# Kernel optimization log

Measured on AMD Instinct MI355X. Metric: run time of the kernel, lower is better.

The kernel has to match this reference:

```python
import jax, jax.numpy as jnp
import numpy as np

H = 4      # SSM / attn heads (d_model/headdim = 256/64)
WIN = 4    # attention window over bands


def _ln(x, g, b):
    m = jnp.mean(x, -1, keepdims=True)
    v = jnp.mean((x - m) ** 2, -1, keepdims=True)
    return (x - m) * jax.lax.rsqrt(v + 1e-5) * g + b


def setup_inputs() -> dict:
    key = jax.random.key(0)
    ks = jax.random.split(key, 24)
    def rn(i, shape, s=0.05):
        return jax.random.normal(ks[i], shape, jnp.float32) * s
    B, T, K, D = 2, 256, 8, 256
    return {
        "z": rn(0, (B, T, K, D), 1.0),
        "ln1_g": jnp.ones((D,), jnp.float32), "ln1_b": jnp.zeros((D,), jnp.float32),
        "Wx": rn(1, (D, D)), "conv_w": rn(2, (D, 4), 0.3), "Wz": rn(3, (D, D)),
        "Wb": rn(4, (D, H * 128)), "Wc": rn(5, (D, H * 128)), "Wdt": rn(6, (D, H)),
        "dt_bias": rn(7, (H,), 0.5), "A_log": rn(8, (H,), 0.5), "theta": rn(9, (H,), 1.0),
        "D_skip": rn(10, (H,), 1.0), "mimo_U": rn(11, (H, H), 0.5), "mimo_V": rn(12, (H, H), 0.5),
        "Wout": rn(13, (D, D)),
        "ln2_g": jnp.ones((D,), jnp.float32), "ln2_b": jnp.zeros((D,), jnp.float32),
        "attn_in_w": rn(14, (3 * D, D)), "attn_in_b": rn(15, (3 * D,), 0.02),
        "attn_out_w": rn(16, (D, D)), "attn_out_b": jnp.zeros((D,), jnp.float32),
        "ln3_g": jnp.ones((D,), jnp.float32), "ln3_b": jnp.zeros((D,), jnp.float32),
        "Wg": rn(17, (D, 4 * D)), "Wu": rn(18, (D, 4 * D)), "Wd": rn(19, (4 * D, D)),
    }


def _forward(z, ln1_g, ln1_b, Wx, conv_w, Wz, Wb, Wc, Wdt, dt_bias, A_log, theta,
             D_skip, mimo_U, mimo_V, Wout, ln2_g, ln2_b, attn_in_w, attn_in_b,
             attn_out_w, attn_out_b, ln3_g, ln3_b, Wg, Wu, Wd):
    B, T, K, D = z.shape
    P = D // H
    N = Wb.shape[1] // H
    # ---------- (a) intra-band Mamba3 (complex MIMO selective scan) ----------
    u = _ln(z, ln1_g, ln1_b)
    u = jnp.transpose(u, (0, 2, 1, 3)).reshape(B * K, T, D)   # [BK,T,D]
    x = u @ Wx
    # causal depthwise conv1d, kernel 4
    xp = jnp.pad(x, ((0, 0), (3, 0), (0, 0)))
    x = sum(xp[:, k:k + T, :] * conv_w[:, k] for k in range(4))
    x = jax.nn.silu(x)
    xh = x.reshape(B * K, T, H, P)
    Bm = (u @ Wb).reshape(B * K, T, H, N)
    Cm = (u @ Wc).reshape(B * K, T, H, N)
    Mmix = mimo_U @ mimo_V.T                                  # rank-r cross-head coupling
    Bm = jnp.einsum('hg,btgn->bthn', Mmix, Bm)
    dt = jax.nn.softplus(u @ Wdt + dt_bias)                   # [BK,T,H]
    A = -jnp.exp(A_log)                                       # stable real decay
    mag = jnp.exp(dt * A)
    ph = dt * theta                                           # harmonic rotation
    ar, ai = mag * jnp.cos(ph), mag * jnp.sin(ph)
    xs = tuple(jnp.moveaxis(t, 1, 0) for t in (xh, Bm, Cm, dt, ar, ai))
    h0 = jnp.zeros((B * K, H, N, P), x.dtype)

    def step(carry, s):
        h_re, h_im = carry
        xt, bt, ct, dtt, art, ait = s
        dBx = (dtt[:, :, None, None] * bt[:, :, :, None]) * xt[:, :, None, :]
        nr = art[:, :, None, None] * h_re - ait[:, :, None, None] * h_im + dBx
        ni = art[:, :, None, None] * h_im + ait[:, :, None, None] * h_re
        return (nr, ni), jnp.einsum('bhn,bhnp->bhp', ct, nr)   # Re(C . h)

    _, ys = jax.lax.scan(step, (h0, h0), xs)                  # ys: [T,BK,H,P]
    y = jnp.moveaxis(ys, 0, 1) + D_skip[None, None, :, None] * xh
    y = y.reshape(B * K, T, D) * jax.nn.silu(u @ Wz)
    y = y @ Wout
    z = z + jnp.transpose(y.reshape(B, K, T, D), (0, 2, 1, 3))
    # ---------- (b) inter-band windowed attention ----------
    zn = _ln(z, ln2_g, ln2_b).reshape(B * T, K, D)
    qkv = zn @ attn_in_w.T + attn_in_b
    q, k_, v = jnp.split(qkv, 3, axis=-1)
    hd = D // H
    def hs(t):
        return t.reshape(B * T, K // WIN, WIN, H, hd).transpose(0, 1, 3, 2, 4)
    q, k_, v = hs(q), hs(k_), hs(v)
    s = jnp.einsum('mwhqd,mwhkd->mwhqk', q, k_) * jnp.float32(1.0 / np.sqrt(hd))
    a = jax.nn.softmax(s, axis=-1)
    o = jnp.einsum('mwhqk,mwhkd->mwhqd', a, v).transpose(0, 1, 3, 2, 4).reshape(B * T, K, D)
    z = z + (o @ attn_out_w.T + attn_out_b).reshape(B, T, K, D)
    # ---------- (c) SwiGLU FFN ----------
    zf = _ln(z, ln3_g, ln3_b)
    z = z + (jax.nn.silu(zf @ Wg) * (zf @ Wu)) @ Wd
    return z


def reference(z, ln1_g, ln1_b, Wx, conv_w, Wz, Wb, Wc, Wdt, dt_bias, A_log, theta,
              D_skip, mimo_U, mimo_V, Wout, ln2_g, ln2_b, attn_in_w, attn_in_b,
              attn_out_w, attn_out_b, ln3_g, ln3_b, Wg, Wu, Wd):
    return _forward(z, ln1_g, ln1_b, Wx, conv_w, Wz, Wb, Wc, Wdt, dt_bias, A_log,
                    theta, D_skip, mimo_U, mimo_V, Wout, ln2_g, ln2_b, attn_in_w,
                    attn_in_b, attn_out_w, attn_out_b, ln3_g, ln3_b, Wg, Wu, Wd)
```

## Files before the change

kernel.cpp:

```cpp
#include <hip/hip_runtime.h>
#include <hip/hip_bf16.h>
#include <math.h>

typedef __hip_bfloat16 bf16;
typedef __attribute__((ext_vector_type(8))) short s16x8;
typedef __attribute__((ext_vector_type(4))) float f32x4;

__device__ __forceinline__ float siluf(float x) { return x / (1.f + __expf(-x)); }
__device__ __forceinline__ float bits2f(unsigned short u) {
    union { float f; unsigned i; } v; v.i = ((unsigned)u) << 16; return v.f;
}
__device__ __forceinline__ unsigned short f2bits(float f) {
    return (unsigned short)__bfloat16_as_ushort(__float2bfloat16(f));
}

#define KFL 1024
#define OFF_UB   (768*KFL)
#define OFF_DTV  (1280*KFL)
#define OFF_BMB  (1344*KFL)
#define OFF_CMB  (2368*KFL)
#define OFF_ZGB  (3392*KFL)
#define OFF_XB   (3904*KFL)
#define OFF_X2T  (4928*KFL)
#define OFF_P    (5440*KFL)
#define OFF_YGB  (7488*KFL)
#define OFF_Z1   (8000*KFL)
#define OFF_ZNB  OFF_UB
#define OFF_QKV  OFF_BMB
#define OFF_OB   (2880*KFL)
#define OFF_Z2   OFF_P
#define OFF_ZFB  (6464*KFL)
#define OFF_GG   OFF_BMB

#define W_BCZX 0
#define W_OUT  393216
#define W_QKV  458752
#define W_AO   655360
#define W_GU   720896
#define W_D    1245184

__global__ __launch_bounds__(256) void prep_ln1_kernel(
    const float* __restrict__ Wx, const float* __restrict__ Wb,
    const float* __restrict__ Wc, const float* __restrict__ Wz,
    const float* __restrict__ Wo, const float* __restrict__ Wqkv,
    const float* __restrict__ Wao, const float* __restrict__ Wg,
    const float* __restrict__ Wu, const float* __restrict__ Wd,
    const float* __restrict__ U, const float* __restrict__ V,
    unsigned short* __restrict__ wout,
    const float* __restrict__ z, const float* __restrict__ g1,
    const float* __restrict__ b1, const float* __restrict__ Wdt,
    const float* __restrict__ dt_bias,
    unsigned short* __restrict__ u, float4* __restrict__ dtv4)
{
    __shared__ __align__(16) float smem[64 * 65];
    int blk = blockIdx.x;
    int tid = threadIdx.x;
    if (blk < 368) {
        if (blk >= 304) {
            int off = blk - 304;
            const float* src; int dst, base;
            if (off < 48) { src = Wqkv; dst = W_QKV; base = off * 4096; }
            else          { src = Wao;  dst = W_AO;  base = (off - 48) * 4096; }
            #pragma unroll
            for (int i = 0; i < 16; i++) {
                int idx = base + tid + i * 256;
                wout[dst + idx] = f2bits(src[idx]);
            }
            return;
        }
        float* lds = smem;
        const float* src; int srcN, n0, sc0, k0, dstoff, dstK, mix = 0, t;
        if (blk < 32)       { t = blk;       src = Wb; srcN = 512;  dstoff = W_BCZX; dstK = 256;
                              n0 = (t >> 2) * 64;        sc0 = 0; k0 = (t & 3) * 64; mix = 1; }
        else if (blk < 64)  { t = blk - 32;  src = Wc; srcN = 512;  dstoff = W_BCZX; dstK = 256;
                              n0 = 512 + (t >> 2) * 64;  sc0 = (t >> 2) * 64; k0 = (t & 3) * 64; }
        else if (blk < 80)  { t = blk - 64;  src = Wz; srcN = 256;  dstoff = W_BCZX; dstK = 256;
                              n0 = 1024 + (t >> 2) * 64; sc0 = (t >> 2) * 64; k0 = (t & 3) * 64; }
        else if (blk < 96)  { t = blk - 80;  src = Wx; srcN = 256;  dstoff = W_BCZX; dstK = 256;
                              n0 = 1280 + (t >> 2) * 64; sc0 = (t >> 2) * 64; k0 = (t & 3) * 64; }
        else if (blk < 112) { t = blk - 96;  src = Wo; srcN = 256;  dstoff = W_OUT;  dstK = 256;
                              n0 = (t >> 2) * 64;        sc0 = n0; k0 = (t & 3) * 64; }
        else if (blk < 176) { t = blk - 112; src = Wg; srcN = 1024; dstoff = W_GU;   dstK = 256;
                              n0 = (t >> 2) * 64;        sc0 = n0; k0 = (t & 3) * 64; }
        else if (blk < 240) { t = blk - 176; src = Wu; srcN = 1024; dstoff = W_GU;   dstK = 256;
                              n0 = 1024 + (t >> 2) * 64; sc0 = (t >> 2) * 64; k0 = (t & 3) * 64; }
        else                { t = blk - 240; src = Wd; srcN = 256;  dstoff = W_D;    dstK = 1024;
                              n0 = (t >> 4) * 64;        sc0 = n0; k0 = (t & 15) * 64; }
        if (mix) {
            int h = n0 >> 7, scol = n0 & 127;
            float mm[4];
            #pragma unroll
            for (int g = 0; g < 4; g++) {
                float s = 0.f;
                #pragma unroll
                for (int j = 0; j < 4; j++) s += U[h * 4 + j] * V[g * 4 + j];
                mm[g] = s;
            }
            #pragma unroll
            for (int i = 0; i < 16; i++) {
                int idx = tid + i * 256;
                int kk = idx >> 6, nn = idx & 63;
                const float* row = src + (size_t)(k0 + kk) * 512 + scol + nn;
                lds[kk * 65 + nn] = mm[0] * row[0] + mm[1] * row[128]
                                  + mm[2] * row[256] + mm[3] * row[384];
            }
        } else {
            #pragma unroll
            for (int i = 0; i < 16; i++) {
                int idx = tid + i * 256;
                int kk = idx >> 6, nn = idx & 63;
                lds[kk * 65 + nn] = src[(size_t)(k0 + kk) * srcN + sc0 + nn];
            }
        }
        __syncthreads();
        #pragma unroll
        for (int i = 0; i < 16; i++) {
            int idx = tid + i * 256;
            int nn = idx >> 6, kk = idx & 63;
            wout[dstoff + (size_t)(n0 + nn) * dstK + k0 + kk] = f2bits(lds[kk * 65 + nn]);
        }
        return;
    }
    int r = blk - 368;
    float* lds = smem;
    float* dts = smem + 4;
    int t = r & 255, bk = r >> 8;
    int b_ = bk >> 3, k = bk & 7;
    int srcr = ((b_ * 256 + t) * 8 + k) * 256;
    int d = tid;
    float x = z[srcr + d];
    float v = x;
    #pragma unroll
    for (int off = 32; off; off >>= 1) v += __shfl_xor(v, off, 64);
    if ((d & 63) == 0) lds[d >> 6] = v;
    __syncthreads();
    float mean = (lds[0] + lds[1] + lds[2] + lds[3]) * (1.f / 256.f);
    __syncthreads();
    float c = x - mean;
    v = c * c;
    #pragma unroll
    for (int off = 32; off; off >>= 1) v += __shfl_xor(v, off, 64);
    if ((d & 63) == 0) lds[d >> 6] = v;
    __syncthreads();
    float var = (lds[0] + lds[1] + lds[2] + lds[3]) * (1.f / 256.f);
    float uval = c * rsqrtf(var + 1e-5f) * g1[d] + b1[d];
    u[r * 256 + d] = f2bits(uval);
    float4 wv = *(const float4*)(Wdt + d * 4);
    float q0 = uval * wv.x, q1 = uval * wv.y, q2 = uval * wv.z, q3 = uval * wv.w;
    #pragma unroll
    for (int off = 32; off; off >>= 1) {
        q0 += __shfl_xor(q0, off, 64);
        q1 += __shfl_xor(q1, off, 64);
        q2 += __shfl_xor(q2, off, 64);
        q3 += __shfl_xor(q3, off, 64);
    }
    if ((d & 63) == 0) {
        int w = d >> 6;
        dts[w * 4 + 0] = q0; dts[w * 4 + 1] = q1;
        dts[w * 4 + 2] = q2; dts[w * 4 + 3] = q3;
    }
    __syncthreads();
    if (d == 0) {
        float dv[4];
        #pragma unroll
        for (int h = 0; h < 4; h++) {
            float xx = dts[h] + dts[4 + h] + dts[8 + h] + dts[12 + h] + dt_bias[h];
            dv[h] = (xx > 20.f) ? xx : log1pf(__expf(xx));
        }
        dtv4[r] = make_float4(dv[0], dv[1], dv[2], dv[3]);
    }
}

__global__ __launch_bounds__(256) void gemm_bczx(
    const unsigned short* __restrict__ A, const unsigned short* __restrict__ Bt,
    unsigned short* __restrict__ bmb, unsigned short* __restrict__ cmb,
    unsigned short* __restrict__ zgb, unsigned short* __restrict__ xb)
{
    __shared__ unsigned short As[128 * 40];
    __shared__ unsigned short Bs[128 * 40];
    const int K = 256;
    int tid = threadIdx.x;
    int n0 = blockIdx.x * 128, m0 = blockIdx.y * 128;
    int w = tid >> 6, l = tid & 63;
    int mwave = (w >> 1) * 64, nwave = (w & 1) * 64;
    f32x4 acc[4][4] = {};
    int srow = tid >> 2, sc = (tid & 3) * 8;
    const unsigned short* Ap = A + (size_t)(m0 + srow) * K + sc;
    const unsigned short* Bp = Bt + (size_t)(n0 + srow) * K + sc;
    int lq = l & 15, lh = l >> 4, ko = lh * 8;
    uint4 a0 = *(const uint4*)(Ap);
    uint4 a1 = *(const uint4*)(Ap + (size_t)64 * K);
    uint4 b0 = *(const uint4*)(Bp);
    uint4 b1 = *(const uint4*)(Bp + (size_t)64 * K);
    for (int k0 = 0; k0 < K; k0 += 32) {
        if (k0) __syncthreads();
        *(uint4*)&As[srow * 40 + sc] = a0;
        *(uint4*)&As[(srow + 64) * 40 + sc] = a1;
        *(uint4*)&Bs[srow * 40 + sc] = b0;
        *(uint4*)&Bs[(srow + 64) * 40 + sc] = b1;
        __syncthreads();
        if (k0 + 32 < K) {
            a0 = *(const uint4*)(Ap + k0 + 32);
            a1 = *(const uint4*)(Ap + (size_t)64 * K + k0 + 32);
            b0 = *(const uint4*)(Bp + k0 + 32);
            b1 = *(const uint4*)(Bp + (size_t)64 * K + k0 + 32);
        }
        s16x8 bfr[4];
        #pragma unroll
        for (int nf = 0; nf < 4; nf++)
            bfr[nf] = *(const s16x8*)&Bs[(nwave + nf * 16 + lq) * 40 + ko];
        #pragma unroll
        for (int mf = 0; mf < 4; mf++) {
            s16x8 af = *(const s16x8*)&As[(mwave + mf * 16 + lq) * 40 + ko];
            #pragma unroll
            for (int nf = 0; nf < 4; nf++)
                acc[mf][nf] = __builtin_amdgcn_mfma_f32_16x16x32_bf16(af, bfr[nf], acc[mf][nf], 0, 0, 0);
        }
    }
    #pragma unroll
    for (int mf = 0; mf < 4; mf++) {
        #pragma unroll
        for (int nf = 0; nf < 4; nf++) {
            int n = n0 + nwave + nf * 16 + lq;
            #pragma unroll
            for (int r = 0; r < 4; r++) {
                int m = m0 + mwave + mf * 16 + lh * 4 + r;
                float v = acc[mf][nf][r];
                if (n < 512)       bmb[(size_t)m * 512 + n] = f2bits(v);
                else if (n < 1024) cmb[(size_t)m * 512 + (n - 512)] = f2bits(v);
                else if (n < 1280) zgb[(size_t)m * 256 + (n - 1024)] = f2bits(siluf(v));
                else               xb[(size_t)m * 256 + (n - 1280)] = f2bits(v);
            }
        }
    }
}

__global__ __launch_bounds__(256) void s_conv_kernel(
    const unsigned short* __restrict__ cmb, const unsigned short* __restrict__ bmb,
    const float4* __restrict__ dtv4, const float* __restrict__ A_log,
    const float* __restrict__ theta, unsigned short* __restrict__ P,
    const unsigned short* __restrict__ xb, const float* __restrict__ cw,
    unsigned short* __restrict__ x2t)
{
    __shared__ __align__(16) char smem[23808];
    int blk = blockIdx.x;
    int tid = threadIdx.x;
    if (blk >= 192) {
        int c = blk - 192;
        int bhid = c >> 2, tt = c & 3;
        int bk = bhid >> 2, h = bhid & 3;
        int t0 = tt * 64;
        float* tile = (float*)smem;
        #pragma unroll
        for (int i = 0; i < 17; i++) {
            int idx = tid + i * 256;
            if (idx < 67 * 64) {
                int tr = idx >> 6, dd = idx & 63;
                int t = t0 - 3 + tr;
                tile[tr * 65 + dd] = (t >= 0)
                    ? bits2f(xb[(size_t)(bk * 256 + t) * 256 + h * 64 + dd]) : 0.f;
            }
        }
        __syncthreads();
        int wv_ = tid >> 6, lt = tid & 63;
        #pragma unroll 4
        for (int pi = 0; pi < 16; pi++) {
            int p = wv_ * 16 + pi;
            float4 wv = *(const float4*)(cw + (h * 64 + p) * 4);
            float acc = tile[lt * 65 + p] * wv.x + tile[(lt + 1) * 65 + p] * wv.y +
                        tile[(lt + 2) * 65 + p] * wv.z + tile[(lt + 3) * 65 + p] * wv.w;
            x2t[(size_t)(bhid * 64 + p) * 256 + t0 + lt] = f2bits(siluf(acc));
        }
        return;
    }
    int map = blk >> 6;
    int bh = blk & 63;
    int bx = (map == 2) ? 1 : 0;
    int by = (map == 0) ? 0 : 1;
    int bk = bh >> 2, h = bh & 3;
    unsigned short* As = (unsigned short*)smem;
    unsigned short* Bs = As + 128 * 40;
    float* mAs = (float*)(smem + 20480);
    float* phs = mAs + 256;
    float* dss = phs + 256;
    {
        float4 dv = dtv4[bk * 256 + tid];
        float dth = (h == 0) ? dv.x : (h == 1) ? dv.y : (h == 2) ? dv.z : dv.w;
        float Ah = -__expf(A_log[h]);
        float th = theta[h];
        dss[tid] = dth;
        mAs[tid] = dth * Ah;
        phs[tid] = dth * th;
        __syncthreads();
        for (int off = 1; off < 256; off <<= 1) {
            float a = 0.f, p = 0.f;
            int use = (tid >= off);
            if (use) { a = mAs[tid - off]; p = phs[tid - off]; }
            __syncthreads();
            if (use) { mAs[tid] += a; phs[tid] += p; }
            __syncthreads();
        }
    }
    int w = tid >> 6, l = tid & 63;
    int mwave = (w >> 1) * 64, nwave = (w & 1) * 64;
    int lq = l & 15, lh = l >> 4, ko = lh * 8;
    unsigned short* Pout = P + (size_t)bh * 65536;
    f32x4 acc[4][4] = {};
    int srow = tid >> 2, sc = (tid & 3) * 8;
    const unsigned short* Ap = cmb + (size_t)(bk * 256 + by * 128 + srow) * 512 + h * 128 + sc;
    const unsigned short* Bp = bmb + (size_t)(bk * 256 + bx * 128 + srow) * 512 + h * 128 + sc;
    uint4 a0 = *(const uint4*)(Ap);
    uint4 a1 = *(const uint4*)(Ap + (size_t)64 * 512);
    uint4 b0 = *(const uint4*)(Bp);
    uint4 b1 = *(const uint4*)(Bp + (size_t)64 * 512);
    for (int k0 = 0; k0 < 128; k0 += 32) {
        __syncthreads();
        *(uint4*)&As[srow * 40 + sc] = a0;
        *(uint4*)&As[(srow + 64) * 40 + sc] = a1;
        *(uint4*)&Bs[srow * 40 + sc] = b0;
        *(uint4*)&Bs[(srow + 64) * 40 + sc] = b1;
        __syncthreads();
        if (k0 + 32 < 128) {
            a0 = *(const uint4*)(Ap + k0 + 32);
            a1 = *(const uint4*)(Ap + (size_t)64 * 512 + k0 + 32);
            b0 = *(const uint4*)(Bp + k0 + 32);
            b1 = *(const uint4*)(Bp + (size_t)64 * 512 + k0 + 32);
        }
        s16x8 bfr[4];
        #pragma unroll
        for (int nf = 0; nf < 4; nf++)
            bfr[nf] = *(const s16x8*)&Bs[(nwave + nf * 16 + lq) * 40 + ko];
        #pragma unroll
        for (int mf = 0; mf < 4; mf++) {
            s16x8 af = *(const s16x8*)&As[(mwave + mf * 16 + lq) * 40 + ko];
            #pragma unroll
            for (int nf = 0; nf < 4; nf++)
                acc[mf][nf] = __builtin_amdgcn_mfma_f32_16x16x32_bf16(af, bfr[nf], acc[mf][nf], 0, 0, 0);
        }
    }
    #pragma unroll
    for (int mf = 0; mf < 4; mf++) {
        float tmv[4], tpv[4]; int tg[4];
        #pragma unroll
        for (int r = 0; r < 4; r++) {
            tg[r] = by * 128 + mwave + mf * 16 + lh * 4 + r;
            tmv[r] = mAs[tg[r]];
            tpv[r] = phs[tg[r]];
        }
        #pragma unroll
        for (int nf = 0; nf < 4; nf++) {
            int s = bx * 128 + nwave + nf * 16 + lq;
            float ms = mAs[s];
            float ps = phs[s];
            float ds = dss[s];
            #pragma unroll
            for (int r = 0; r < 4; r++) {
                float wgt = (s <= tg[r])
                    ? __expf(tmv[r] - ms) * __cosf(tpv[r] - ps) * ds : 0.f;
                Pout[tg[r] * 256 + s] = f2bits(acc[mf][nf][r] * wgt);
            }
        }
    }
}

__global__ __launch_bounds__(256) void gemm_y(
    const unsigned short* __restrict__ P, const unsigned short* __restrict__ x2t,
    const unsigned short* __restrict__ zgb, const float* __restrict__ Dsk,
    unsigned short* __restrict__ ygb)
{
    int by = blockIdx.x, bh = blockIdx.y;
    int bk = bh >> 2, h = bh & 3;
    int tid = threadIdx.x;
    int w = tid >> 6, l = tid & 63;
    int mw = (w >> 1) * 32, nw = (w & 1) * 32;
    int lq = l & 15, lh = l >> 4, ko = lh * 8;
    __shared__ unsigned short As[64 * 40];
    __shared__ unsigned short Bs[64 * 40];
    f32x4 acc[2][2] = {};
    int srow = tid >> 2, sc = (tid & 3) * 8;
    const unsigned short* Ap = P + (size_t)bh * 65536 + (size_t)(by * 64 + srow) * 256 + sc;
    const unsigned short* Bp = x2t + (size_t)bh * 16384 + (size_t)srow * 256 + sc;
    int kmax = (by + 1) * 64; if (kmax > 256) kmax = 256;
    uint4 a0 = *(const uint4*)(Ap);
    uint4 b0 = *(const uint4*)(Bp);
    for (int k0 = 0; k0 < kmax; k0 += 32) {
        if (k0) __syncthreads();
        *(uint4*)&As[srow * 40 + sc] = a0;
        *(uint4*)&Bs[srow * 40 + sc] = b0;
        __syncthreads();
        if (k0 + 32 < kmax) {
            a0 = *(const uint4*)(Ap + k0 + 32);
            b0 = *(const uint4*)(Bp + k0 + 32);
        }
        s16x8 bfr[2];
        #pragma unroll
        for (int nf = 0; nf < 2; nf++)
            bfr[nf] = *(const s16x8*)&Bs[(nw + nf * 16 + lq) * 40 + ko];
        #pragma unroll
        for (int mf = 0; mf < 2; mf++) {
            s16x8 af = *(const s16x8*)&As[(mw + mf * 16 + lq) * 40 + ko];
            #pragma unroll
            for (int nf = 0; nf < 2; nf++)
                acc[mf][nf] = __builtin_amdgcn_mfma_f32_16x16x32_bf16(af, bfr[nf], acc[mf][nf], 0, 0, 0);
        }
    }
    float dsk = Dsk[h];
    #pragma unroll
    for (int mf = 0; mf < 2; mf++) {
        #pragma unroll
        for (int nf = 0; nf < 2; nf++) {
            int p = nw + nf * 16 + lq;
            #pragma unroll
            for (int r = 0; r < 4; r++) {
                int t = by * 64 + mw + mf * 16 + lh * 4 + r;
                float xv = bits2f(x2t[(size_t)bh * 16384 + p * 256 + t]);
                float zg = bits2f(zgb[(size_t)(bk * 256 + t) * 256 + h * 64 + p]);
                ygb[(size_t)(bk * 256 + t) * 256 + h * 64 + p] =
                    f2bits((acc[mf][nf][r] + dsk * xv) * zg);
            }
        }
    }
}

__global__ __launch_bounds__(256) void gemm_ln(
    const unsigned short* __restrict__ A, const unsigned short* __restrict__ Bt,
    const float* __restrict__ bias, const float* __restrict__ resid,
    const float* __restrict__ g, const float* __restrict__ b,
    float* __restrict__ zfull, unsigned short* __restrict__ znorm, int rowmap)
{
    const int K = 256;
    __shared__ unsigned short As[16 * 40];
    __shared__ unsigned short Bs[256 * 40];
    __shared__ float partS[16][4], partQ[16][4];
    int tid = threadIdx.x;
    int m0 = blockIdx.x * 16;
    int w = tid >> 6, l = tid & 63;
    int nw = w * 64;
    int lq = l & 15, lh = l >> 4, ko = lh * 8;
    f32x4 acc[4] = {};
    int srow = tid >> 2, sc = (tid & 3) * 8;
    const unsigned short* Ap = A + (size_t)(m0 + (srow & 15)) * K + sc;
    const unsigned short* Bp = Bt + (size_t)srow * K + sc;
    uint4 a0 = *(const uint4*)(Ap);
    uint4 b0 = *(const uint4*)(Bp);
    uint4 b1 = *(const uint4*)(Bp + (size_t)64 * K);
    uint4 b2 = *(const uint4*)(Bp + (size_t)128 * K);
    uint4 b3 = *(const uint4*)(Bp + (size_t)192 * K);
    for (int k0 = 0; k0 < K; k0 += 32) {
        if (k0) __syncthreads();
        if (tid < 64) *(uint4*)&As[srow * 40 + sc] = a0;
        *(uint4*)&Bs[srow * 40 + sc] = b0;
        *(uint4*)&Bs[(srow + 64) * 40 + sc] = b1;
        *(uint4*)&Bs[(srow + 128) * 40 + sc] = b2;
        *(uint4*)&Bs[(srow + 192) * 40 + sc] = b3;
        __syncthreads();
        if (k0 + 32 < K) {
            a0 = *(const uint4*)(Ap + k0 + 32);
            b0 = *(const uint4*)(Bp + k0 + 32);
            b1 = *(const uint4*)(Bp + (size_t)64 * K + k0 + 32);
            b2 = *(const uint4*)(Bp + (size_t)128 * K + k0 + 32);
            b3 = *(const uint4*)(Bp + (size_t)192 * K + k0 + 32);
        }
        s16x8 af = *(const s16x8*)&As[lq * 40 + ko];
        #pragma unroll
        for (int nf = 0; nf < 4; nf++) {
            s16x8 bf = *(const s16x8*)&Bs[(nw + nf * 16 + lq) * 40 + ko];
            acc[nf] = __builtin_amdgcn_mfma_f32_16x16x32_bf16(af, bf, acc[nf], 0, 0, 0);
        }
    }
    float bv[4];
    #pragma unroll
    for (int nf = 0; nf < 4; nf++) bv[nf] = bias ? bias[nw + nf * 16 + lq] : 0.f;
    int orow[4];
    #pragma unroll
    for (int r = 0; r < 4; r++) {
        int rb = m0 + lh * 4 + r;
        if (rowmap) {
            int bk = rb >> 8, t = rb & 255;
            orow[r] = ((bk >> 3) * 256 + t) * 8 + (bk & 7);
        } else orow[r] = rb;
    }
    #pragma unroll
    for (int r = 0; r < 4; r++) {
        float s = 0.f, q = 0.f;
        #pragma unroll
        for (int nf = 0; nf < 4; nf++) {
            float v = acc[nf][r] + bv[nf]
                    + resid[(size_t)orow[r] * 256 + nw + nf * 16 + lq];
            acc[nf][r] = v;
            s += v; q += v * v;
        }
        #pragma unroll
        for (int off = 1; off < 16; off <<= 1) {
            s += __shfl_xor(s, off, 64);
            q += __shfl_xor(q, off, 64);
        }
        if (lq == 0) {
            int row = lh * 4 + r;
            partS[row][w] = s; partQ[row][w] = q;
        }
    }
    __syncthreads();
    float gv[4], bbv[4];
    #pragma unroll
    for (int nf = 0; nf < 4; nf++) {
        gv[nf] = g[nw + nf * 16 + lq];
        bbv[nf] = b[nw + nf * 16 + lq];
    }
    #pragma unroll
    for (int r = 0; r < 4; r++) {
        int row = lh * 4 + r;
        float sum = partS[row][0] + partS[row][1] + partS[row][2] + partS[row][3];
        float sq  = partQ[row][0] + partQ[row][1] + partQ[row][2] + partQ[row][3];
        float mean = sum * (1.f / 256.f);
        float var = sq * (1.f / 256.f) - mean * mean;
        float rstd = rsqrtf(var + 1e-5f);
        size_t ro = (size_t)orow[r] * 256;
        #pragma unroll
        for (int nf = 0; nf < 4; nf++) {
            int n = nw + nf * 16 + lq;
            float v = acc[nf][r];
            zfull[ro + n] = v;
            znorm[ro + n] = f2bits((v - mean) * rstd * gv[nf] + bbv[nf]);
        }
    }
}

__global__ __launch_bounds__(256) void mfma_gemm(
    const unsigned short* __restrict__ A, const unsigned short* __restrict__ Bt,
    const float* __restrict__ bias, void* __restrict__ C,
    int N, int K, int out_bf16)
{
    __shared__ unsigned short As[128 * 40];
    __shared__ unsigned short Bs[128 * 40];
    int tid = threadIdx.x;
    int n0 = blockIdx.x * 128, m0 = blockIdx.y * 128;
    int w = tid >> 6, l = tid & 63;
    int mwave = (w >> 1) * 64, nwave = (w & 1) * 64;
    f32x4 acc[4][4] = {};
    int srow = tid >> 2, sc = (tid & 3) * 8;
    const unsigned short* Ap = A + (size_t)(m0 + srow) * K + sc;
    const unsigned short* Bp = Bt + (size_t)(n0 + srow) * K + sc;
    int lq = l & 15, lh = l >> 4, ko = lh * 8;
    uint4 a0 = *(const uint4*)(Ap);
    uint4 a1 = *(const uint4*)(Ap + (size_t)64 * K);
    uint4 b0 = *(const uint4*)(Bp);
    uint4 b1 = *(const uint4*)(Bp + (size_t)64 * K);
    for (int k0 = 0; k0 < K; k0 += 32) {
        if (k0) __syncthreads();
        *(uint4*)&As[srow * 40 + sc] = a0;
        *(uint4*)&As[(srow + 64) * 40 + sc] = a1;
        *(uint4*)&Bs[srow * 40 + sc] = b0;
        *(uint4*)&Bs[(srow + 64) * 40 + sc] = b1;
        __syncthreads();
        if (k0 + 32 < K) {
            a0 = *(const uint4*)(Ap + k0 + 32);
            a1 = *(const uint4*)(Ap + (size_t)64 * K + k0 + 32);
            b0 = *(const uint4*)(Bp + k0 + 32);
            b1 = *(const uint4*)(Bp + (size_t)64 * K + k0 + 32);
        }
        s16x8 bfr[4];
        #pragma unroll
        for (int nf = 0; nf < 4; nf++)
            bfr[nf] = *(const s16x8*)&Bs[(nwave + nf * 16 + lq) * 40 + ko];
        #pragma unroll
        for (int mf = 0; mf < 4; mf++) {
            s16x8 af = *(const s16x8*)&As[(mwave + mf * 16 + lq) * 40 + ko];
            #pragma unroll
            for (int nf = 0; nf < 4; nf++)
                acc[mf][nf] = __builtin_amdgcn_mfma_f32_16x16x32_bf16(af, bfr[nf], acc[mf][nf], 0, 0, 0);
        }
    }
    #pragma unroll
    for (int mf = 0; mf < 4; mf++) {
        #pragma unroll
        for (int nf = 0; nf < 4; nf++) {
            int n = n0 + nwave + nf * 16 + lq;
            float bs_ = bias ? bias[n] : 0.f;
            #pragma unroll
            for (int r = 0; r < 4; r++) {
                int m = m0 + mwave + mf * 16 + lh * 4 + r;
                float v = acc[mf][nf][r] + bs_;
                if (out_bf16) ((unsigned short*)C)[(size_t)m * N + n] = f2bits(v);
                else          ((float*)C)[(size_t)m * N + n] = v;
            }
        }
    }
}

__global__ __launch_bounds__(256) void gemm_gu2(
    const unsigned short* __restrict__ A, const unsigned short* __restrict__ Wgu,
    unsigned short* __restrict__ gg)
{
    const int K = 256;
    __shared__ unsigned short As[128 * 40];
    __shared__ unsigned short Bgs[64 * 40];
    __shared__ unsigned short Bus[64 * 40];
    int tid = threadIdx.x;
    int n0 = blockIdx.x * 64, m0 = blockIdx.y * 128;
    int w = tid >> 6, l = tid & 63;
    int mwave = (w >> 1) * 64, nwave = (w & 1) * 32;
    int lq = l & 15, lh = l >> 4, ko = lh * 8;
    f32x4 ag[4][2] = {}, au[4][2] = {};
    int srow = tid >> 2, sc = (tid & 3) * 8;
    const unsigned short* Ap = A + (size_t)(m0 + srow) * K + sc;
    const unsigned short* Bgp = Wgu + (size_t)(n0 + srow) * K + sc;
    const unsigned short* Bup = Wgu + (size_t)(1024 + n0 + srow) * K + sc;
    uint4 a0 = *(const uint4*)(Ap);
    uint4 a1 = *(const uint4*)(Ap + (size_t)64 * K);
    uint4 bg = *(const uint4*)(Bgp);
    uint4 bu = *(const uint4*)(Bup);
    for (int k0 = 0; k0 < K; k0 += 32) {
        if (k0) __syncthreads();
        *(uint4*)&As[srow * 40 + sc] = a0;
        *(uint4*)&As[(srow + 64) * 40 + sc] = a1;
        *(uint4*)&Bgs[srow * 40 + sc] = bg;
        *(uint4*)&Bus[srow * 40 + sc] = bu;
        __syncthreads();
        if (k0 + 32 < K) {
            a0 = *(const uint4*)(Ap + k0 + 32);
            a1 = *(const uint4*)(Ap + (size_t)64 * K + k0 + 32);
            bg = *(const uint4*)(Bgp + k0 + 32);
            bu = *(const uint4*)(Bup + k0 + 32);
        }
        s16x8 bgr[2], bur[2];
        #pragma unroll
        for (int nf = 0; nf < 2; nf++) {
            bgr[nf] = *(const s16x8*)&Bgs[(nwave + nf * 16 + lq) * 40 + ko];
            bur[nf] = *(const s16x8*)&Bus[(nwave + nf * 16 + lq) * 40 + ko];
        }
        #pragma unroll
        for (int mf = 0; mf < 4; mf++) {
            s16x8 af = *(const s16x8*)&As[(mwave + mf * 16 + lq) * 40 + ko];
            #pragma unroll
            for (int nf = 0; nf < 2; nf++) {
                ag[mf][nf] = __builtin_amdgcn_mfma_f32_16x16x32_bf16(af, bgr[nf], ag[mf][nf], 0, 0, 0);
                au[mf][nf] = __builtin_amdgcn_mfma_f32_16x16x32_bf16(af, bur[nf], au[mf][nf], 0, 0, 0);
            }
        }
    }
    #pragma unroll
    for (int mf = 0; mf < 4; mf++) {
        #pragma unroll
        for (int nf = 0; nf < 2; nf++) {
            int n = n0 + nwave + nf * 16 + lq;
            #pragma unroll
            for (int r = 0; r < 4; r++) {
                int m = m0 + mwave + mf * 16 + lh * 4 + r;
                gg[(size_t)m * 1024 + n] = f2bits(siluf(ag[mf][nf][r]) * au[mf][nf][r]);
            }
        }
    }
}

__global__ __launch_bounds__(256) void gemm_d2(
    const unsigned short* __restrict__ gg, const unsigned short* __restrict__ Bt,
    const float* __restrict__ resid, float* __restrict__ out)
{
    __shared__ unsigned short As[64 * 40];
    __shared__ unsigned short Bs[64 * 40];
    const int K = 1024, N = 256;
    int tid = threadIdx.x;
    int n0 = blockIdx.x * 64, m0 = blockIdx.y * 64;
    int w = tid >> 6, l = tid & 63;
    int mw = (w >> 1) * 32, nw = (w & 1) * 32;
    f32x4 acc[2][2] = {};
    int srow = tid >> 2, sc = (tid & 3) * 8;
    const unsigned short* Ap = gg + (size_t)(m0 + srow) * K + sc;
    const unsigned short* Bp = Bt + (size_t)(n0 + srow) * K + sc;
    int lq = l & 15, lh = l >> 4, ko = lh * 8;
    uint4 a0 = *(const uint4*)(Ap);
    uint4 b0 = *(const uint4*)(Bp);
    for (int k0 = 0; k0 < K; k0 += 32) {
        if (k0) __syncthreads();
        *(uint4*)&As[srow * 40 + sc] = a0;
        *(uint4*)&Bs[srow * 40 + sc] = b0;
        __syncthreads();
        if (k0 + 32 < K) {
            a0 = *(const uint4*)(Ap + k0 + 32);
            b0 = *(const uint4*)(Bp + k0 + 32);
        }
        s16x8 bfr[2];
        #pragma unroll
        for (int nf = 0; nf < 2; nf++)
            bfr[nf] = *(const s16x8*)&Bs[(nw + nf * 16 + lq) * 40 + ko];
        #pragma unroll
        for (int mf = 0; mf < 2; mf++) {
            s16x8 af = *(const s16x8*)&As[(mw + mf * 16 + lq) * 40 + ko];
            #pragma unroll
            for (int nf = 0; nf < 2; nf++)
                acc[mf][nf] = __builtin_amdgcn_mfma_f32_16x16x32_bf16(af, bfr[nf], acc[mf][nf], 0, 0, 0);
        }
    }
    #pragma unroll
    for (int mf = 0; mf < 2; mf++) {
        #pragma unroll
        for (int nf = 0; nf < 2; nf++) {
            int n = n0 + nw + nf * 16 + lq;
            #pragma unroll
            for (int r = 0; r < 4; r++) {
                int m = m0 + mw + mf * 16 + lh * 4 + r;
                out[(size_t)m * N + n] = acc[mf][nf][r] + resid[(size_t)m * N + n];
            }
        }
    }
}

__global__ __launch_bounds__(256) void attn_kernel(const unsigned short* __restrict__ qkv,
    unsigned short* __restrict__ o)
{
    int m = blockIdx.x >> 1, w = blockIdx.x & 1;
    int tid = threadIdx.x;
    int h = tid >> 6, d = tid & 63;
    __shared__ float qs[4][256], ks[4][256], vs[4][256];
    #pragma unroll
    for (int j = 0; j < 4; j++) {
        int row = m * 8 + w * 4 + j;
        int base = row * 768;
        qs[j][tid] = bits2f(qkv[base + tid]);
        ks[j][tid] = bits2f(qkv[base + 256 + tid]);
        vs[j][tid] = bits2f(qkv[base + 512 + tid]);
    }
    __syncthreads();
    float sc[4][4];
    #pragma unroll
    for (int qi = 0; qi < 4; qi++)
        #pragma unroll
        for (int ki = 0; ki < 4; ki++) {
            float v = qs[qi][h * 64 + d] * ks[ki][h * 64 + d];
            #pragma unroll
            for (int off = 32; off; off >>= 1) v += __shfl_xor(v, off, 64);
            sc[qi][ki] = v * 0.125f;
        }
    #pragma unroll
    for (int qi = 0; qi < 4; qi++) {
        float mx = fmaxf(fmaxf(sc[qi][0], sc[qi][1]), fmaxf(sc[qi][2], sc[qi][3]));
        float e0 = __expf(sc[qi][0] - mx), e1 = __expf(sc[qi][1] - mx);
        float e2 = __expf(sc[qi][2] - mx), e3 = __expf(sc[qi][3] - mx);
        float inv = 1.f / (e0 + e1 + e2 + e3);
        float ov = (e0 * vs[0][h * 64 + d] + e1 * vs[1][h * 64 + d] +
                    e2 * vs[2][h * 64 + d] + e3 * vs[3][h * 64 + d]) * inv;
        o[(m * 8 + w * 4 + qi) * 256 + h * 64 + d] = f2bits(ov);
    }
}

extern "C" void kernel_launch(void* const* d_in, const int* in_sizes, int n_in,
                              void* d_out, int out_size, void* d_ws, size_t ws_size,
                              hipStream_t stream)
{
    const float* z         = (const float*)d_in[0];
    const float* ln1_g     = (const float*)d_in[1];
    const float* ln1_b     = (const float*)d_in[2];
    const float* Wx        = (const float*)d_in[3];
    const float* conv_w    = (const float*)d_in[4];
    const float* Wz        = (const float*)d_in[5];
    const float* Wb        = (const float*)d_in[6];
    const float* Wc        = (const float*)d_in[7];
    const float* Wdt       = (const float*)d_in[8];
    const float* dt_bias   = (const float*)d_in[9];
    const float* A_log     = (const float*)d_in[10];
    const float* theta     = (const float*)d_in[11];
    const float* D_skip    = (const float*)d_in[12];
    const float* mimo_U    = (const float*)d_in[13];
    const float* mimo_V    = (const float*)d_in[14];
    const float* Wout      = (const float*)d_in[15];
    const float* ln2_g     = (const float*)d_in[16];
    const float* ln2_b     = (const float*)d_in[17];
    const float* attn_in_w = (const float*)d_in[18];
    const float* attn_in_b = (const float*)d_in[19];
    const float* attn_out_w= (const float*)d_in[20];
    const float* attn_out_b= (const float*)d_in[21];
    const float* ln3_g     = (const float*)d_in[22];
    const float* ln3_b     = (const float*)d_in[23];
    const float* Wg        = (const float*)d_in[24];
    const float* Wu        = (const float*)d_in[25];
    const float* Wd        = (const float*)d_in[26];

    float* W = (float*)d_ws;
    unsigned short* wts = (unsigned short*)W;
    unsigned short* ub  = (unsigned short*)(W + OFF_UB);
    float4* dtv4        = (float4*)(W + OFF_DTV);
    unsigned short* bmb = (unsigned short*)(W + OFF_BMB);
    unsigned short* cmb = (unsigned short*)(W + OFF_CMB);
    unsigned short* zgb = (unsigned short*)(W + OFF_ZGB);
    unsigned short* xb  = (unsigned short*)(W + OFF_XB);
    unsigned short* x2t = (unsigned short*)(W + OFF_X2T);
    unsigned short* pbuf= (unsigned short*)(W + OFF_P);
    unsigned short* ygb = (unsigned short*)(W + OFF_YGB);
    float* z1           = W + OFF_Z1;
    unsigned short* znb = (unsigned short*)(W + OFF_ZNB);
    unsigned short* qkvb= (unsigned short*)(W + OFF_QKV);
    unsigned short* ob  = (unsigned short*)(W + OFF_OB);
    float* z2           = W + OFF_Z2;
    unsigned short* zfb = (unsigned short*)(W + OFF_ZFB);
    unsigned short* gg  = (unsigned short*)(W + OFF_GG);

    prep_ln1_kernel<<<4464, 256, 0, stream>>>(
        Wx, Wb, Wc, Wz, Wout, attn_in_w, attn_out_w, Wg, Wu, Wd, mimo_U, mimo_V,
        wts, z, ln1_g, ln1_b, Wdt, dt_bias, ub, dtv4);
    gemm_bczx<<<dim3(12, 32), 256, 0, stream>>>(ub, wts + W_BCZX, bmb, cmb, zgb, xb);
    s_conv_kernel<<<448, 256, 0, stream>>>(cmb, bmb, dtv4, A_log, theta, pbuf,
                                           xb, conv_w, x2t);
    gemm_y<<<dim3(4, 64), 256, 0, stream>>>(pbuf, x2t, zgb, D_skip, ygb);
    gemm_ln<<<256, 256, 0, stream>>>(ygb, wts + W_OUT, nullptr, z, ln2_g, ln2_b,
                                     z1, znb, 1);
    mfma_gemm<<<dim3(6, 32), 256, 0, stream>>>(znb, wts + W_QKV, attn_in_b, qkvb, 768, 256, 1);
    attn_kernel<<<1024, 256, 0, stream>>>(qkvb, ob);
    gemm_ln<<<256, 256, 0, stream>>>(ob, wts + W_AO, attn_out_b, z1, ln3_g, ln3_b,
                                     z2, zfb, 0);
    gemm_gu2<<<dim3(16, 32), 256, 0, stream>>>(zfb, wts + W_GU, gg);
    gemm_d2<<<dim3(4, 64), 256, 0, stream>>>(gg, wts + W_D, z2, (float*)d_out);
}
```

Measured before the change: 215.7 us.

## Fuse SSM output GEMM into out-proj LN and attention into attn-out LN

```diff
diff --git a/kernel.cpp b/kernel.cpp
--- a/kernel.cpp
+++ b/kernel.cpp
@@ -23,11 +23,9 @@
 #define OFF_XB   (3904*KFL)
 #define OFF_X2T  (4928*KFL)
 #define OFF_P    (5440*KFL)
-#define OFF_YGB  (7488*KFL)
 #define OFF_Z1   (8000*KFL)
 #define OFF_ZNB  OFF_UB
 #define OFF_QKV  OFF_BMB
-#define OFF_OB   (2880*KFL)
 #define OFF_Z2   OFF_P
 #define OFF_ZFB  (6464*KFL)
 #define OFF_GG   OFF_BMB
@@ -363,130 +361,80 @@
     }
 }
 
-__global__ __launch_bounds__(256) void gemm_y(
+__global__ __launch_bounds__(256) void gemm_yln(
     const unsigned short* __restrict__ P, const unsigned short* __restrict__ x2t,
     const unsigned short* __restrict__ zgb, const float* __restrict__ Dsk,
-    unsigned short* __restrict__ ygb)
+    const unsigned short* __restrict__ Wo, const float* __restrict__ resid,
+    const float* __restrict__ g, const float* __restrict__ b,
+    float* __restrict__ z1, unsigned short* __restrict__ znb)
 {
-    int by = blockIdx.x, bh = blockIdx.y;
-    int bk = bh >> 2, h = bh & 3;
-    int tid = threadIdx.x;
-    int w = tid >> 6, l = tid & 63;
-    int mw = (w >> 1) * 32, nw = (w & 1) * 32;
-    int lq = l & 15, lh = l >> 4, ko = lh * 8;
-    __shared__ unsigned short As[64 * 40];
-    __shared__ unsigned short Bs[64 * 40];
-    f32x4 acc[2][2] = {};
-    int srow = tid >> 2, sc = (tid & 3) * 8;
-    const unsigned short* Ap = P + (size_t)bh * 65536 + (size_t)(by * 64 + srow) * 256 + sc;
-    const unsigned short* Bp = x2t + (size_t)bh * 16384 + (size_t)srow * 256 + sc;
-    int kmax = (by + 1) * 64; if (kmax > 256) kmax = 256;
-    uint4 a0 = *(const uint4*)(Ap);
-    uint4 b0 = *(const uint4*)(Bp);
-    for (int k0 = 0; k0 < kmax; k0 += 32) {
-        if (k0) __syncthreads();
-        *(uint4*)&As[srow * 40 + sc] = a0;
-        *(uint4*)&Bs[srow * 40 + sc] = b0;
-        __syncthreads();
-        if (k0 + 32 < kmax) {
-            a0 = *(const uint4*)(Ap + k0 + 32);
-            b0 = *(const uint4*)(Bp + k0 + 32);
-        }
-        s16x8 bfr[2];
-        #pragma unroll
-        for (int nf = 0; nf < 2; nf++)
-            bfr[nf] = *(const s16x8*)&Bs[(nw + nf * 16 + lq) * 40 + ko];
-        #pragma unroll
-        for (int mf = 0; mf < 2; mf++) {
-            s16x8 af = *(const s16x8*)&As[(mw + mf * 16 + lq) * 40 + ko];
-            #pragma unroll
-            for (int nf = 0; nf < 2; nf++)
-                acc[mf][nf] = __builtin_amdgcn_mfma_f32_16x16x32_bf16(af, bfr[nf], acc[mf][nf], 0, 0, 0);
-        }
-    }
-    float dsk = Dsk[h];
-    #pragma unroll
-    for (int mf = 0; mf < 2; mf++) {
-        #pragma unroll
-        for (int nf = 0; nf < 2; nf++) {
-            int p = nw + nf * 16 + lq;
-            #pragma unroll
-            for (int r = 0; r < 4; r++) {
-                int t = by * 64 + mw + mf * 16 + lh * 4 + r;
-                float xv = bits2f(x2t[(size_t)bh * 16384 + p * 256 + t]);
-                float zg = bits2f(zgb[(size_t)(bk * 256 + t) * 256 + h * 64 + p]);
-                ygb[(size_t)(bk * 256 + t) * 256 + h * 64 + p] =
-                    f2bits((acc[mf][nf][r] + dsk * xv) * zg);
-            }
-        }
-    }
-}
-
-__global__ __launch_bounds__(256) void gemm_ln(
-    const unsigned short* __restrict__ A, const unsigned short* __restrict__ Bt,
-    const float* __restrict__ bias, const float* __restrict__ resid,
-    const float* __restrict__ g, const float* __restrict__ b,
-    float* __restrict__ zfull, unsigned short* __restrict__ znorm, int rowmap)
-{
-    const int K = 256;
-    __shared__ unsigned short As[16 * 40];
+    __shared__ unsigned short As3[16 * 40];
+    __shared__ unsigned short Bs3[64 * 40];
+    __shared__ unsigned short As2[16 * 280];
     __shared__ unsigned short Bs[256 * 40];
     __shared__ float partS[16][4], partQ[16][4];
     int tid = threadIdx.x;
     int m0 = blockIdx.x * 16;
-    int w = tid >> 6, l = tid & 63;
-    int nw = w * 64;
+    int bk = m0 >> 8, t0 = m0 & 255;
+    int wv = tid >> 6, l = tid & 63;
     int lq = l & 15, lh = l >> 4, ko = lh * 8;
+    int srow = tid >> 2, sc = (tid & 3) * 8;
+    int kmaxy = (t0 + 16 + 31) & ~31; if (kmaxy > 256) kmaxy = 256;
+    for (int h = 0; h < 4; h++) {
+        int bh = bk * 4 + h;
+        f32x4 acc = {};
+        const unsigned short* Ap = P + (size_t)bh * 65536 + (size_t)(t0 + (srow & 15)) * 256 + sc;
+        const unsigned short* Bp = x2t + (size_t)bh * 16384 + (size_t)srow * 256 + sc;
+        for (int k0 = 0; k0 < kmaxy; k0 += 32) {
+            __syncthreads();
+            if (tid < 64) *(uint4*)&As3[srow * 40 + sc] = *(const uint4*)(Ap + k0);
+            *(uint4*)&Bs3[srow * 40 + sc] = *(const uint4*)(Bp + k0);
+            __syncthreads();
+            s16x8 af = *(const s16x8*)&As3[lq * 40 + ko];
+            s16x8 bf = *(const s16x8*)&Bs3[(wv * 16 + lq) * 40 + ko];
+            acc = __builtin_amdgcn_mfma_f32_16x16x32_bf16(af, bf, acc, 0, 0, 0);
+        }
+        float dsk = Dsk[h];
+        int p = wv * 16 + lq;
+        #pragma unroll
+        for (int r = 0; r < 4; r++) {
+            int tr = lh * 4 + r;
+            float xv = bits2f(x2t[(size_t)bh * 16384 + p * 256 + t0 + tr]);
+            float zg = bits2f(zgb[(size_t)(m0 + tr) * 256 + h * 64 + p]);
+            As2[tr * 280 + h * 64 + p] = f2bits((acc[r] + dsk * xv) * zg);
+        }
+    }
+    const int K = 256;
     f32x4 acc[4] = {};
-    int srow = tid >> 2, sc = (tid & 3) * 8;
-    const unsigned short* Ap = A + (size_t)(m0 + (srow & 15)) * K + sc;
-    const unsigned short* Bp = Bt + (size_t)srow * K + sc;
-    uint4 a0 = *(const uint4*)(Ap);
-    uint4 b0 = *(const uint4*)(Bp);
-    uint4 b1 = *(const uint4*)(Bp + (size_t)64 * K);
-    uint4 b2 = *(const uint4*)(Bp + (size_t)128 * K);
-    uint4 b3 = *(const uint4*)(Bp + (size_t)192 * K);
+    const unsigned short* Bp = Wo + (size_t)srow * K + sc;
+    int nw = wv * 64;
     for (int k0 = 0; k0 < K; k0 += 32) {
-        if (k0) __syncthreads();
-        if (tid < 64) *(uint4*)&As[srow * 40 + sc] = a0;
-        *(uint4*)&Bs[srow * 40 + sc] = b0;
-        *(uint4*)&Bs[(srow + 64) * 40 + sc] = b1;
-        *(uint4*)&Bs[(srow + 128) * 40 + sc] = b2;
-        *(uint4*)&Bs[(srow + 192) * 40 + sc] = b3;
-        __syncthreads();
-        if (k0 + 32 < K) {
-            a0 = *(const uint4*)(Ap + k0 + 32);
-            b0 = *(const uint4*)(Bp + k0 + 32);
-            b1 = *(const uint4*)(Bp + (size_t)64 * K + k0 + 32);
-            b2 = *(const uint4*)(Bp + (size_t)128 * K + k0 + 32);
-            b3 = *(const uint4*)(Bp + (size_t)192 * K + k0 + 32);
-        }
-        s16x8 af = *(const s16x8*)&As[lq * 40 + ko];
+        __syncthreads();
+        *(uint4*)&Bs[srow * 40 + sc] = *(const uint4*)(Bp + k0);
+        *(uint4*)&Bs[(srow + 64) * 40 + sc] = *(const uint4*)(Bp + (size_t)64 * K + k0);
+        *(uint4*)&Bs[(srow + 128) * 40 + sc] = *(const uint4*)(Bp + (size_t)128 * K + k0);
+        *(uint4*)&Bs[(srow + 192) * 40 + sc] = *(const uint4*)(Bp + (size_t)192 * K + k0);
+        __syncthreads();
+        s16x8 af = *(const s16x8*)&As2[lq * 280 + k0 + ko];
         #pragma unroll
         for (int nf = 0; nf < 4; nf++) {
             s16x8 bf = *(const s16x8*)&Bs[(nw + nf * 16 + lq) * 40 + ko];
             acc[nf] = __builtin_amdgcn_mfma_f32_16x16x32_bf16(af, bf, acc[nf], 0, 0, 0);
         }
     }
-    float bv[4];
-    #pragma unroll
-    for (int nf = 0; nf < 4; nf++) bv[nf] = bias ? bias[nw + nf * 16 + lq] : 0.f;
     int orow[4];
     #pragma unroll
     for (int r = 0; r < 4; r++) {
         int rb = m0 + lh * 4 + r;
-        if (rowmap) {
-            int bk = rb >> 8, t = rb & 255;
-            orow[r] = ((bk >> 3) * 256 + t) * 8 + (bk & 7);
-        } else orow[r] = rb;
+        int t = rb & 255;
+        orow[r] = ((bk >> 3) * 256 + t) * 8 + (bk & 7);
     }
     #pragma unroll
     for (int r = 0; r < 4; r++) {
         float s = 0.f, q = 0.f;
         #pragma unroll
         for (int nf = 0; nf < 4; nf++) {
-            float v = acc[nf][r] + bv[nf]
-                    + resid[(size_t)orow[r] * 256 + nw + nf * 16 + lq];
+            float v = acc[nf][r] + resid[(size_t)orow[r] * 256 + nw + nf * 16 + lq];
             acc[nf][r] = v;
             s += v; q += v * v;
         }
@@ -497,7 +445,7 @@
         }
         if (lq == 0) {
             int row = lh * 4 + r;
-            partS[row][w] = s; partQ[row][w] = q;
+            partS[row][wv] = s; partQ[row][wv] = q;
         }
     }
     __syncthreads();
@@ -520,8 +468,8 @@
         for (int nf = 0; nf < 4; nf++) {
             int n = nw + nf * 16 + lq;
             float v = acc[nf][r];
-            zfull[ro + n] = v;
-            znorm[ro + n] = f2bits((v - mean) * rstd * gv[nf] + bbv[nf]);
+            z1[ro + n] = v;
+            znb[ro + n] = f2bits((v - mean) * rstd * gv[nf] + bbv[nf]);
         }
     }
 }
@@ -584,6 +532,133 @@
                 if (out_bf16) ((unsigned short*)C)[(size_t)m * N + n] = f2bits(v);
                 else          ((float*)C)[(size_t)m * N + n] = v;
             }
+        }
+    }
+}
+
+__global__ __launch_bounds__(256) void gemm_attn_ln(
+    const unsigned short* __restrict__ qkv, const unsigned short* __restrict__ Wao,
+    const float* __restrict__ bias, const float* __restrict__ resid,
+    const float* __restrict__ g, const float* __restrict__ b,
+    float* __restrict__ z2, unsigned short* __restrict__ zfb)
+{
+    __shared__ unsigned short qs[16 * 784];
+    __shared__ unsigned short As2[16 * 280];
+    __shared__ unsigned short Bs[256 * 40];
+    __shared__ float partS[16][4], partQ[16][4];
+    int tid = threadIdx.x;
+    int m0 = blockIdx.x * 16;
+    int wv = tid >> 6, l = tid & 63;
+    int lq = l & 15, lh = l >> 4, ko = lh * 8;
+    int srow = tid >> 2, sc = (tid & 3) * 8;
+    #pragma unroll
+    for (int i = 0; i < 8; i++) {
+        int idx = tid + i * 256;
+        int r = idx >> 7, c = idx & 127;
+        if (c < 96)
+            *(uint4*)&qs[r * 784 + c * 8] =
+                *(const uint4*)(qkv + (size_t)(m0 + r) * 768 + c * 8);
+    }
+    __syncthreads();
+    {
+        int h = l >> 4, q16 = l & 15;
+        int rb = wv * 4;
+        float scr[4][4];
+        #pragma unroll
+        for (int qi = 0; qi < 4; qi++) {
+            #pragma unroll
+            for (int ki = 0; ki < 4; ki++) {
+                const unsigned short* qp = &qs[(rb + qi) * 784 + h * 64 + q16 * 4];
+                const unsigned short* kp = &qs[(rb + ki) * 784 + 256 + h * 64 + q16 * 4];
+                float pv = bits2f(qp[0]) * bits2f(kp[0]) + bits2f(qp[1]) * bits2f(kp[1])
+                         + bits2f(qp[2]) * bits2f(kp[2]) + bits2f(qp[3]) * bits2f(kp[3]);
+                pv += __shfl_xor(pv, 1, 64);
+                pv += __shfl_xor(pv, 2, 64);
+                pv += __shfl_xor(pv, 4, 64);
+                pv += __shfl_xor(pv, 8, 64);
+                scr[qi][ki] = pv * 0.125f;
+            }
+        }
+        #pragma unroll
+        for (int qi = 0; qi < 4; qi++) {
+            float mx = fmaxf(fmaxf(scr[qi][0], scr[qi][1]), fmaxf(scr[qi][2], scr[qi][3]));
+            float e0 = __expf(scr[qi][0] - mx), e1 = __expf(scr[qi][1] - mx);
+            float e2 = __expf(scr[qi][2] - mx), e3 = __expf(scr[qi][3] - mx);
+            float inv = 1.f / (e0 + e1 + e2 + e3);
+            #pragma unroll
+            for (int j = 0; j < 4; j++) {
+                int dd = h * 64 + q16 * 4 + j;
+                float ov = (e0 * bits2f(qs[(rb + 0) * 784 + 512 + dd])
+                          + e1 * bits2f(qs[(rb + 1) * 784 + 512 + dd])
+                          + e2 * bits2f(qs[(rb + 2) * 784 + 512 + dd])
+                          + e3 * bits2f(qs[(rb + 3) * 784 + 512 + dd])) * inv;
+                As2[(rb + qi) * 280 + dd] = f2bits(ov);
+            }
+        }
+    }
+    const int K = 256;
+    f32x4 acc[4] = {};
+    const unsigned short* Bp = Wao + (size_t)srow * K + sc;
+    int nw = wv * 64;
+    for (int k0 = 0; k0 < K; k0 += 32) {
+        __syncthreads();
+        *(uint4*)&Bs[srow * 40 + sc] = *(const uint4*)(Bp + k0);
+        *(uint4*)&Bs[(srow + 64) * 40 + sc] = *(const uint4*)(Bp + (size_t)64 * K + k0);
+        *(uint4*)&Bs[(srow + 128) * 40 + sc] = *(const uint4*)(Bp + (size_t)128 * K + k0);
+        *(uint4*)&Bs[(srow + 192) * 40 + sc] = *(const uint4*)(Bp + (size_t)192 * K + k0);
+        __syncthreads();
+        s16x8 af = *(const s16x8*)&As2[lq * 280 + k0 + ko];
+        #pragma unroll
+        for (int nf = 0; nf < 4; nf++) {
+            s16x8 bf = *(const s16x8*)&Bs[(nw + nf * 16 + lq) * 40 + ko];
+            acc[nf] = __builtin_amdgcn_mfma_f32_16x16x32_bf16(af, bf, acc[nf], 0, 0, 0);
+        }
+    }
+    float bv[4];
+    #pragma unroll
+    for (int nf = 0; nf < 4; nf++) bv[nf] = bias ? bias[nw + nf * 16 + lq] : 0.f;
+    #pragma unroll
+    for (int r = 0; r < 4; r++) {
+        int m = m0 + lh * 4 + r;
+        float s = 0.f, q = 0.f;
+        #pragma unroll
+        for (int nf = 0; nf < 4; nf++) {
+            float v = acc[nf][r] + bv[nf] + resid[(size_t)m * 256 + nw + nf * 16 + lq];
+            acc[nf][r] = v;
+            s += v; q += v * v;
+        }
+        #pragma unroll
+        for (int off = 1; off < 16; off <<= 1) {
+            s += __shfl_xor(s, off, 64);
+            q += __shfl_xor(q, off, 64);
+        }
+        if (lq == 0) {
+            int row = lh * 4 + r;
+            partS[row][wv] = s; partQ[row][wv] = q;
+        }
+    }
+    __syncthreads();
+    float gv[4], bbv[4];
+    #pragma unroll
+    for (int nf = 0; nf < 4; nf++) {
+        gv[nf] = g[nw + nf * 16 + lq];
+        bbv[nf] = b[nw + nf * 16 + lq];
+    }
+    #pragma unroll
+    for (int r = 0; r < 4; r++) {
+        int row = lh * 4 + r;
+        int m = m0 + row;
+        float sum = partS[row][0] + partS[row][1] + partS[row][2] + partS[row][3];
+        float sq  = partQ[row][0] + partQ[row][1] + partQ[row][2] + partQ[row][3];
+        float mean = sum * (1.f / 256.f);
+        float var = sq * (1.f / 256.f) - mean * mean;
+        float rstd = rsqrtf(var + 1e-5f);
+        #pragma unroll
+        for (int nf = 0; nf < 4; nf++) {
+            int n = nw + nf * 16 + lq;
+            float v = acc[nf][r];
+            z2[(size_t)m * 256 + n] = v;
+            zfb[(size_t)m * 256 + n] = f2bits((v - mean) * rstd * gv[nf] + bbv[nf]);
         }
     }
 }
@@ -703,44 +778,6 @@
                 out[(size_t)m * N + n] = acc[mf][nf][r] + resid[(size_t)m * N + n];
             }
         }
-    }
-}
-
-__global__ __launch_bounds__(256) void attn_kernel(const unsigned short* __restrict__ qkv,
-    unsigned short* __restrict__ o)
-{
-    int m = blockIdx.x >> 1, w = blockIdx.x & 1;
-    int tid = threadIdx.x;
-    int h = tid >> 6, d = tid & 63;
-    __shared__ float qs[4][256], ks[4][256], vs[4][256];
-    #pragma unroll
-    for (int j = 0; j < 4; j++) {
-        int row = m * 8 + w * 4 + j;
-        int base = row * 768;
-        qs[j][tid] = bits2f(qkv[base + tid]);
-        ks[j][tid] = bits2f(qkv[base + 256 + tid]);
-        vs[j][tid] = bits2f(qkv[base + 512 + tid]);
-    }
-    __syncthreads();
-    float sc[4][4];
-    #pragma unroll
-    for (int qi = 0; qi < 4; qi++)
-        #pragma unroll
-        for (int ki = 0; ki < 4; ki++) {
-            float v = qs[qi][h * 64 + d] * ks[ki][h * 64 + d];
-            #pragma unroll
-            for (int off = 32; off; off >>= 1) v += __shfl_xor(v, off, 64);
-            sc[qi][ki] = v * 0.125f;
-        }
-    #pragma unroll
-    for (int qi = 0; qi < 4; qi++) {
-        float mx = fmaxf(fmaxf(sc[qi][0], sc[qi][1]), fmaxf(sc[qi][2], sc[qi][3]));
-        float e0 = __expf(sc[qi][0] - mx), e1 = __expf(sc[qi][1] - mx);
-        float e2 = __expf(sc[qi][2] - mx), e3 = __expf(sc[qi][3] - mx);
-        float inv = 1.f / (e0 + e1 + e2 + e3);
-        float ov = (e0 * vs[0][h * 64 + d] + e1 * vs[1][h * 64 + d] +
-                    e2 * vs[2][h * 64 + d] + e3 * vs[3][h * 64 + d]) * inv;
-        o[(m * 8 + w * 4 + qi) * 256 + h * 64 + d] = f2bits(ov);
     }
 }
 
@@ -786,11 +823,9 @@
     unsigned short* xb  = (unsigned short*)(W + OFF_XB);
     unsigned short* x2t = (unsigned short*)(W + OFF_X2T);
     unsigned short* pbuf= (unsigned short*)(W + OFF_P);
-    unsigned short* ygb = (unsigned short*)(W + OFF_YGB);
     float* z1           = W + OFF_Z1;
     unsigned short* znb = (unsigned short*)(W + OFF_ZNB);
     unsigned short* qkvb= (unsigned short*)(W + OFF_QKV);
-    unsigned short* ob  = (unsigned short*)(W + OFF_OB);
     float* z2           = W + OFF_Z2;
     unsigned short* zfb = (unsigned short*)(W + OFF_ZFB);
     unsigned short* gg  = (unsigned short*)(W + OFF_GG);
@@ -801,13 +836,11 @@
     gemm_bczx<<<dim3(12, 32), 256, 0, stream>>>(ub, wts + W_BCZX, bmb, cmb, zgb, xb);
     s_conv_kernel<<<448, 256, 0, stream>>>(cmb, bmb, dtv4, A_log, theta, pbuf,
                                            xb, conv_w, x2t);
-    gemm_y<<<dim3(4, 64), 256, 0, stream>>>(pbuf, x2t, zgb, D_skip, ygb);
-    gemm_ln<<<256, 256, 0, stream>>>(ygb, wts + W_OUT, nullptr, z, ln2_g, ln2_b,
-                                     z1, znb, 1);
+    gemm_yln<<<256, 256, 0, stream>>>(pbuf, x2t, zgb, D_skip, wts + W_OUT, z,
+                                      ln2_g, ln2_b, z1, znb);
     mfma_gemm<<<dim3(6, 32), 256, 0, stream>>>(znb, wts + W_QKV, attn_in_b, qkvb, 768, 256, 1);
-    attn_kernel<<<1024, 256, 0, stream>>>(qkvb, ob);
-    gemm_ln<<<256, 256, 0, stream>>>(ob, wts + W_AO, attn_out_b, z1, ln3_g, ln3_b,
-                                     z2, zfb, 0);
+    gemm_attn_ln<<<256, 256, 0, stream>>>(qkvb, wts + W_AO, attn_out_b, z1,
+                                          ln3_g, ln3_b, z2, zfb);
     gemm_gu2<<<dim3(16, 32), 256, 0, stream>>>(zfb, wts + W_GU, gg);
     gemm_d2<<<dim3(4, 64), 256, 0, stream>>>(gg, wts + W_D, z2, (float*)d_out);
 }
```

Result: slower. 245.5 us (+13.8%).
